# Optimization experiments

Hardware: AMD Instinct MI355X
Metric: run time of the kernel (lower is better)

## Reference

```python
import jax, jax.numpy as jnp
import numpy as np

B, D, N0, N1 = 2, 512, 2048, 2048
ATT_DIM, OUT_DIM, H = 512, 512, 8
HEAD_ATT = ATT_DIM // H   # 64
HEAD_OUT = OUT_DIM // H   # 64
TEMP = 1.0
MASK_FILL = -10000000.0


def setup_inputs() -> dict:
    key = jax.random.key(0)
    ks = jax.random.split(key, 12)
    s = 0.02
    return {
        "feats_query": jax.random.normal(ks[0], (B, D, N0), dtype=jnp.float32),
        "feats_key": jax.random.normal(ks[1], (B, D, N1), dtype=jnp.float32),
        "key_mask": jax.random.randint(ks[2], (B, 1, N1), 0, 2, dtype=jnp.int32),
        # 1x1 Conv1d weights == (out_ch, in_ch) matrices
        "Wq": jax.random.normal(ks[3], (ATT_DIM, D), dtype=jnp.float32) * s,
        "bq": jnp.zeros((ATT_DIM,), dtype=jnp.float32),
        "Wk": jax.random.normal(ks[4], (ATT_DIM, D), dtype=jnp.float32) * s,
        "bk": jnp.zeros((ATT_DIM,), dtype=jnp.float32),
        "Wf": jax.random.normal(ks[5], (OUT_DIM, D), dtype=jnp.float32) * s,
        "bf": jnp.zeros((OUT_DIM,), dtype=jnp.float32),
        "Wm": jax.random.normal(ks[6], (OUT_DIM, OUT_DIM), dtype=jnp.float32) * s,
        "bm": jnp.zeros((OUT_DIM,), dtype=jnp.float32),
        "ln_g": jnp.ones((OUT_DIM,), dtype=jnp.float32),
        "ln_b": jnp.zeros((OUT_DIM,), dtype=jnp.float32),
    }


def _conv1x1(W, b, x):  # x: (b, in, n) -> (b, out, n)
    return jnp.einsum('oi,bin->bon', W, x) + b[None, :, None]


def reference(feats_query, feats_key, key_mask, Wq, bq, Wk, bk, Wf, bf, Wm, bm, ln_g, ln_b):
    b = feats_query.shape[0]
    n0 = feats_query.shape[2]
    n1 = feats_key.shape[2]
    # projections; channel split is (head_dim, head_num) per torch reshape
    q = _conv1x1(Wq, bq, feats_query).reshape(b, HEAD_ATT, H, n0)
    k = _conv1x1(Wk, bk, feats_key).reshape(b, HEAD_ATT, H, n1)
    v = _conv1x1(Wf, bf, feats_key).reshape(b, HEAD_OUT, H, n1)
    # attention: scores scaled by head_att_dim ** 0.5 (dim = query.shape[1])
    scores = jnp.einsum('bdhn,bdhm->bhnm', q / TEMP, k) / (HEAD_ATT ** 0.5)
    mask = key_mask.reshape(b, 1, 1, n1)
    scores = jnp.where(mask == 0, MASK_FILL, scores)
    prob = jax.nn.softmax(scores, axis=-1)
    feats_out = jnp.einsum('bhnm,bdhm->bdhn', prob, v).reshape(b, HEAD_OUT * H, n0)
    feats_out = _conv1x1(Wm, bm, feats_out)
    feats_out = feats_out + feats_query  # skip connection
    # SpecialLayerNorm: layernorm over channel dim (permute 0,2,1 -> LN -> permute back)
    x = feats_out.transpose(0, 2, 1)  # (b, n0, c)
    mu = jnp.mean(x, axis=-1, keepdims=True)
    var = jnp.var(x, axis=-1, keepdims=True)
    x = (x - mu) / jnp.sqrt(var + 1e-5) * ln_g + ln_b
    return x.transpose(0, 2, 1)  # (b, c, n0)
```

## Files before the change

kernel.cpp:

```cpp
#include <hip/hip_runtime.h>
#include <hip/hip_bf16.h>


using bf16x8 = __attribute__((ext_vector_type(8))) __bf16;
using f32x4  = __attribute__((ext_vector_type(4))) float;
using f32x16 = __attribute__((ext_vector_type(16))) float;
using us8    = __attribute__((ext_vector_type(8))) unsigned short;
using u32x4  = __attribute__((ext_vector_type(4))) unsigned int;

__device__ __forceinline__ unsigned short f2b(float f) {
  unsigned int u = __builtin_bit_cast(unsigned int, f);
  u += 0x7fffu + ((u >> 16) & 1u);
  return (unsigned short)(u >> 16);
}
__device__ __forceinline__ float b2f(unsigned short s) {
  unsigned int u = ((unsigned int)s) << 16;
  return __builtin_bit_cast(float, u);
}
__device__ __forceinline__ unsigned int cvtpk(float lo, float hi) {
  unsigned int w;
  asm("v_cvt_pk_bf16_f32 %0, %1, %2" : "=v"(w) : "v"(lo), "v"(hi));
  return w;
}
__device__ __forceinline__ void gl_lds16(const void* g, void* l) {
  __builtin_amdgcn_global_load_lds((const __attribute__((address_space(1))) void*)g,
                                   (__attribute__((address_space(3))) void*)l, 16, 0, 0);
}

__global__ __launch_bounds__(256) void k_transpose(
    const float* __restrict__ fq, const float* __restrict__ fk,
    unsigned short* __restrict__ xqt, unsigned short* __restrict__ xkt)
{
  const int which = blockIdx.z >> 1;
  const int b = blockIdx.z & 1;
  const int i0 = blockIdx.y * 64, n0 = blockIdx.x * 64;
  const float* __restrict__ src = which ? fk : fq;
  unsigned short* __restrict__ dst = which ? xkt : xqt;
  __shared__ float tile[64][65];
  const int t = threadIdx.x;
  const int cl = t & 63, rw = t >> 6;
  #pragma unroll
  for (int rr = 0; rr < 16; ++rr) {
    int il = rr * 4 + rw;
    tile[il][cl] = src[((size_t)b * 512 + i0 + il) * 2048 + n0 + cl];
  }
  __syncthreads();
  #pragma unroll
  for (int rr = 0; rr < 16; ++rr) {
    int nl = rr * 4 + rw;
    dst[((size_t)b * 2048 + n0 + nl) * 512 + i0 + cl] = f2b(tile[cl][nl]);
  }
}

__global__ __launch_bounds__(256) void k_prepw(
    const float* __restrict__ Wq, const float* __restrict__ Wk,
    const float* __restrict__ Wf, const float* __restrict__ Wm,
    const int* __restrict__ mask,
    unsigned short* __restrict__ wqb, unsigned short* __restrict__ wkb,
    unsigned short* __restrict__ wfb, unsigned short* __restrict__ wmb,
    float* __restrict__ biasf)
{
  const int cp = blockIdx.x;
  const int mat = blockIdx.y;
  const int t = threadIdx.x;
  if (mat < 3) {
    const float* W = (mat == 0) ? Wq : (mat == 1) ? Wk : Wf;
    unsigned short* O = (mat == 0) ? wqb : (mat == 1) ? wkb : wfb;
    const int orig = (cp & 63) * 8 + (cp >> 6);
    for (int j = t; j < 512; j += 256)
      O[cp * 512 + j] = f2b(W[orig * 512 + j]);
  } else if (mat == 3) {
    for (int j = t; j < 512; j += 256) {
      int h = j >> 6, d = j & 63;
      wmb[cp * 512 + j] = f2b(Wm[cp * 512 + d * 8 + h]);
    }
  } else {
    if (cp < 16) {
      int i = cp * 256 + t;
      biasf[i] = mask[i] ? 0.f : -100000.f;
    }
  }
}

__device__ __forceinline__ void gemm_tile_128(
    const unsigned short* __restrict__ A,
    const unsigned short* __restrict__ Bt,
    f32x4 (&acc)[4][4])
{
  __shared__ __attribute__((aligned(16))) unsigned short As[128 * 64];
  __shared__ __attribute__((aligned(16))) unsigned short Bs[128 * 64];
  const int t = threadIdx.x;
  const int w = t >> 6, l = t & 63, q = l >> 4, m16 = l & 15;
  const int wm = w >> 1, wn = w & 1;
  const f32x4 fz = {0.f, 0.f, 0.f, 0.f};
  #pragma unroll
  for (int mf = 0; mf < 4; ++mf)
    #pragma unroll
    for (int nf = 0; nf < 4; ++nf) acc[mf][nf] = fz;

  for (int ks = 0; ks < 8; ++ks) {
    __syncthreads();
    #pragma unroll
    for (int i = 0; i < 4; ++i) {
      int s = i * 256 + t;
      int row = s >> 3, j = s & 7;
      int jj = j ^ (row & 7);
      *(us8*)&As[row * 64 + (jj << 3)] = *(const us8*)&A[(size_t)row * 512 + ks * 64 + j * 8];
      *(us8*)&Bs[row * 64 + (jj << 3)] = *(const us8*)&Bt[(size_t)row * 512 + ks * 64 + j * 8];
    }
    __syncthreads();
    #pragma unroll
    for (int kk = 0; kk < 2; ++kk) {
      bf16x8 av[4], bv[4];
      #pragma unroll
      for (int mf = 0; mf < 4; ++mf) {
        int row = wm * 64 + mf * 16 + m16;
        av[mf] = *(const bf16x8*)&As[row * 64 + (((kk * 4 + q) ^ (row & 7)) << 3)];
      }
      #pragma unroll
      for (int nf = 0; nf < 4; ++nf) {
        int row = wn * 64 + nf * 16 + m16;
        bv[nf] = *(const bf16x8*)&Bs[row * 64 + (((kk * 4 + q) ^ (row & 7)) << 3)];
      }
      #pragma unroll
      for (int mf = 0; mf < 4; ++mf)
        #pragma unroll
        for (int nf = 0; nf < 4; ++nf)
          acc[mf][nf] = __builtin_amdgcn_mfma_f32_16x16x32_bf16(av[mf], bv[nf], acc[mf][nf], 0, 0, 0);
    }
  }
}

__global__ __launch_bounds__(256) void k_proj(
    const unsigned short* __restrict__ xqt, const unsigned short* __restrict__ xkt,
    const unsigned short* __restrict__ wqp, const unsigned short* __restrict__ wkp,
    const unsigned short* __restrict__ wfp,
    const float* __restrict__ bq, const float* __restrict__ bk, const float* __restrict__ bfv,
    unsigned short* __restrict__ Qb, unsigned short* __restrict__ Kb, unsigned short* __restrict__ VTb)
{
  const int lid = blockIdx.x;
  const int orig = (lid & 7) * 48 + (lid >> 3);
  const int z = orig >> 6;
  const int bid = orig & 63;
  const int b = z / 3, proj = z % 3;
  const int t = threadIdx.x, w = t >> 6, l = t & 63, q = l >> 4, m16 = l & 15;
  const int wm = w >> 1, wn = w & 1;
  f32x4 acc[4][4];

  const unsigned short* A;
  const unsigned short* Bt;
  int mt, nt_;
  if (proj < 2) {
    mt = bid >> 2; nt_ = bid & 3;
    A  = (proj == 0 ? xqt : xkt) + (size_t)b * 2048 * 512 + (size_t)mt * 128 * 512;
    Bt = (proj == 0 ? wqp : wkp) + (size_t)nt_ * 128 * 512;
  } else {
    mt = bid & 3; nt_ = bid >> 2;
    A  = wfp + (size_t)mt * 128 * 512;
    Bt = xkt + (size_t)b * 2048 * 512 + (size_t)nt_ * 128 * 512;
  }
  gemm_tile_128(A, Bt, acc);

  const float QSCALE = 0.18033688011112042f;

  if (proj < 2) {
    const float* bias = (proj == 0) ? bq : bk;
    unsigned short* dst = (proj == 0) ? Qb : Kb;
    #pragma unroll
    for (int mf = 0; mf < 4; ++mf)
      #pragma unroll
      for (int nf = 0; nf < 4; ++nf)
        #pragma unroll
        for (int r = 0; r < 4; ++r) {
          int n  = mt * 128 + wm * 64 + mf * 16 + q * 4 + r;
          int cp = nt_ * 128 + wn * 64 + nf * 16 + m16;
          int h = cp >> 6, d = cp & 63;
          float v = acc[mf][nf][r] + bias[d * 8 + h];
          if (proj == 0) v *= QSCALE;
          dst[((size_t)(b * 8 + h) * 2048 + n) * 64 + d] = f2b(v);
        }
  } else {
    #pragma unroll
    for (int mf = 0; mf < 4; ++mf)
      #pragma unroll
      for (int nf = 0; nf < 4; ++nf)
        #pragma unroll
        for (int r = 0; r < 4; ++r) {
          int cp = mt * 128 + wm * 64 + mf * 16 + q * 4 + r;
          int n  = nt_ * 128 + wn * 64 + nf * 16 + m16;
          int h = cp >> 6, d = cp & 63;
          float v = acc[mf][nf][r] + bfv[d * 8 + h];
          VTb[((size_t)(b * 8 + h) * 64 + d) * 2048 + n] = f2b(v);
        }
  }
}

__global__ __launch_bounds__(256, 2) void k_attn2(
    const unsigned short* __restrict__ Qb, const unsigned short* __restrict__ Kb,
    const unsigned short* __restrict__ VTb, const float* __restrict__ biasf,
    unsigned short* __restrict__ OT)
{
  const int lid = blockIdx.x;
  const int orig = ((lid & 7) << 6) | (lid >> 3);
  const int bh = orig >> 5, b = bh >> 3, h = bh & 7;
  const int nt = orig & 31;
  const int t = threadIdx.x, w = t >> 6, l = t & 63;
  const int q31 = l & 31, hi = l >> 5;

  __shared__ __attribute__((aligned(16))) char lds_all[65536];
  char* kbuf = lds_all + w * 8192;
  char* vbuf = lds_all + 32768 + w * 8192;

  const unsigned short* Kp = Kb + (size_t)bh * (2048 * 64);
  const unsigned short* Vp = VTb + (size_t)bh * (64 * 2048);
  const float* brow = biasf + b * 2048;

  bf16x8 qfr[2][4];
  {
    const unsigned short* Qp = Qb + ((size_t)bh * 2048 + nt * 64) * 64;
    #pragma unroll
    for (int qf = 0; qf < 2; ++qf)
      #pragma unroll
      for (int tq = 0; tq < 4; ++tq)
        qfr[qf][tq] = *(const bf16x8*)&Qp[(qf * 32 + q31) * 64 + tq * 16 + hi * 8];
  }

  f32x16 oacc[2][2];
  #pragma unroll
  for (int i = 0; i < 2; ++i)
    #pragma unroll
    for (int j2 = 0; j2 < 2; ++j2)
      #pragma unroll
      for (int r = 0; r < 16; ++r) oacc[i][j2][r] = 0.f;
  float lpart[2] = {0.f, 0.f};

  const int kr3 = l >> 3, ks3 = l & 7;
  const int vr4 = l >> 2, vs2 = l & 3;

  {
    int kv0 = w * 32;
    #pragma unroll
    for (int j = 0; j < 4; ++j)
      gl_lds16(Kp + (size_t)(kv0 + j * 8 + kr3) * 64 + (ks3 ^ kr3) * 8, kbuf + j * 1024);
    #pragma unroll
    for (int j = 0; j < 4; ++j) {
      int d = j * 16 + vr4;
      gl_lds16(Vp + (size_t)d * 2048 + kv0 + (vs2 ^ (d & 3)) * 8, vbuf + j * 1024);
    }
  }

  #pragma unroll 2
  for (int i = 0; i < 16; ++i) {
    const int bufi = i & 1;
    const int kv0 = (w + 4 * i) * 32;

    float4 bias[4];
    #pragma unroll
    for (int g = 0; g < 4; ++g)
      bias[g] = *(const float4*)&brow[kv0 + g * 8 + hi * 4];

    if (i < 15) {
      const int kvn = (w + 4 * (i + 1)) * 32;
      char* kb2 = kbuf + (bufi ^ 1) * 4096;
      char* vb2 = vbuf + (bufi ^ 1) * 4096;
      #pragma unroll
      for (int j = 0; j < 4; ++j)
        gl_lds16(Kp + (size_t)(kvn + j * 8 + kr3) * 64 + (ks3 ^ kr3) * 8, kb2 + j * 1024);
      #pragma unroll
      for (int j = 0; j < 4; ++j) {
        int d = j * 16 + vr4;
        gl_lds16(Vp + (size_t)d * 2048 + kvn + (vs2 ^ (d & 3)) * 8, vb2 + j * 1024);
      }
      asm volatile("s_waitcnt vmcnt(8)" ::: "memory");
    } else {
      asm volatile("s_waitcnt vmcnt(0)" ::: "memory");
    }
    __builtin_amdgcn_sched_barrier(0);

    const char* kb = kbuf + bufi * 4096;
    const char* vb = vbuf + bufi * 4096;

    bf16x8 ak[4];
    #pragma unroll
    for (int tq = 0; tq < 4; ++tq)
      ak[tq] = *(const bf16x8*)(kb + q31 * 128 + ((((tq << 1) | hi) ^ (q31 & 7)) * 16));

    f32x16 sacc[2];
    #pragma unroll
    for (int qf = 0; qf < 2; ++qf)
      #pragma unroll
      for (int r = 0; r < 16; ++r) sacc[qf][r] = 0.f;
    #pragma unroll
    for (int tq = 0; tq < 4; ++tq) {
      sacc[0] = __builtin_amdgcn_mfma_f32_32x32x16_bf16(ak[tq], qfr[0][tq], sacc[0], 0, 0, 0);
      sacc[1] = __builtin_amdgcn_mfma_f32_32x32x16_bf16(ak[tq], qfr[1][tq], sacc[1], 0, 0, 0);
    }

    bf16x8 av[2][2];
    #pragma unroll
    for (int df = 0; df < 2; ++df)
      #pragma unroll
      for (int tt = 0; tt < 2; ++tt)
        av[df][tt] = *(const bf16x8*)(vb + (df * 32 + q31) * 64 + ((((tt << 1) | hi) ^ (q31 & 3)) * 16));

    #pragma unroll
    for (int qf = 0; qf < 2; ++qf) {
      float e[16];
      #pragma unroll
      for (int g = 0; g < 4; ++g) {
        e[g*4+0] = __builtin_amdgcn_exp2f(sacc[qf][g*4+0] + bias[g].x);
        e[g*4+1] = __builtin_amdgcn_exp2f(sacc[qf][g*4+1] + bias[g].y);
        e[g*4+2] = __builtin_amdgcn_exp2f(sacc[qf][g*4+2] + bias[g].z);
        e[g*4+3] = __builtin_amdgcn_exp2f(sacc[qf][g*4+3] + bias[g].w);
      }
      float s0 = 0.f;
      #pragma unroll
      for (int r = 0; r < 16; ++r) s0 += e[r];
      lpart[qf] += s0;

      unsigned int W[8];
      #pragma unroll
      for (int j = 0; j < 8; ++j) W[j] = cvtpk(e[2*j], e[2*j+1]);
      asm("v_permlane32_swap_b32 %0, %1" : "+v"(W[0]), "+v"(W[2]));
      asm("v_permlane32_swap_b32 %0, %1" : "+v"(W[1]), "+v"(W[3]));
      asm("v_permlane32_swap_b32 %0, %1" : "+v"(W[4]), "+v"(W[6]));
      asm("v_permlane32_swap_b32 %0, %1" : "+v"(W[5]), "+v"(W[7]));
      u32x4 lo4 = {W[0], W[1], W[2], W[3]};
      u32x4 hi4 = {W[4], W[5], W[6], W[7]};
      bf16x8 pb0 = __builtin_bit_cast(bf16x8, lo4);
      bf16x8 pb1 = __builtin_bit_cast(bf16x8, hi4);

      oacc[0][qf] = __builtin_amdgcn_mfma_f32_32x32x16_bf16(av[0][0], pb0, oacc[0][qf], 0, 0, 0);
      oacc[0][qf] = __builtin_amdgcn_mfma_f32_32x32x16_bf16(av[0][1], pb1, oacc[0][qf], 0, 0, 0);
      oacc[1][qf] = __builtin_amdgcn_mfma_f32_32x32x16_bf16(av[1][0], pb0, oacc[1][qf], 0, 0, 0);
      oacc[1][qf] = __builtin_amdgcn_mfma_f32_32x32x16_bf16(av[1][1], pb1, oacc[1][qf], 0, 0, 0);
    }
  }

  unsigned short* ot = (unsigned short*)kbuf;
  #pragma unroll
  for (int qf = 0; qf < 2; ++qf) {
    float ls = lpart[qf] + __shfl_xor(lpart[qf], 32);
    float rinv = __builtin_amdgcn_rcpf(ls);
    int qq = qf * 32 + q31;
    #pragma unroll
    for (int df = 0; df < 2; ++df)
      #pragma unroll
      for (int rg = 0; rg < 4; ++rg)
        #pragma unroll
        for (int pr = 0; pr < 2; ++pr) {
          int r0 = rg * 4 + pr * 2;
          unsigned int wv = cvtpk(oacc[df][qf][r0] * rinv, oacc[df][qf][r0 + 1] * rinv);
          *(unsigned int*)((char*)ot + qq * 128 + (((df * 4 + rg) ^ (qq & 7)) * 16) + hi * 8 + pr * 4) = wv;
        }
  }
  #pragma unroll
  for (int j = 0; j < 8; ++j) {
    int qq = j * 8 + (l >> 3);
    int sl = l & 7;
    us8 val = *(const us8*)((const char*)ot + qq * 128 + ((sl ^ (qq & 7)) * 16));
    *(us8*)&OT[((size_t)b * 2048 + nt * 64 + qq) * 512 + h * 64 + sl * 8] = val;
  }
}

__global__ __launch_bounds__(256) void k_out(
    const unsigned short* __restrict__ OT, const unsigned short* __restrict__ wmw,
    const float* __restrict__ bm, const unsigned short* __restrict__ xqt,
    const float* __restrict__ g, const float* __restrict__ be,
    float* __restrict__ out)
{
  const int b = blockIdx.y;
  const int n0 = blockIdx.x * 32;
  const int t = threadIdx.x, w = t >> 6, l = t & 63, q = l >> 4, m16 = l & 15;

  __shared__ __attribute__((aligned(16))) unsigned short As[32 * 64];
  __shared__ __attribute__((aligned(16))) unsigned short Bs[4][128 * 64];
  __shared__ float ssum[4][32], ssq[4][32];

  f32x4 acc[2][8];
  const f32x4 fz = {0.f, 0.f, 0.f, 0.f};
  #pragma unroll
  for (int mf = 0; mf < 2; ++mf)
    #pragma unroll
    for (int nf = 0; nf < 8; ++nf) acc[mf][nf] = fz;

  const unsigned short* Abase = OT + ((size_t)b * 2048 + n0) * 512;
  const unsigned short* Bbase = wmw + (size_t)w * 128 * 512;

  const int arow = t >> 3, aj = t & 7;
  for (int ks = 0; ks < 8; ++ks) {
    __syncthreads();
    gl_lds16(Abase + (size_t)arow * 512 + ks * 64 + ((aj ^ (arow & 7)) * 8),
             (char*)As + (size_t)w * 1024);
    #pragma unroll
    for (int c = 0; c < 16; ++c) {
      int slot = c * 64 + l;
      int row = slot >> 3, j = slot & 7;
      gl_lds16(Bbase + (size_t)row * 512 + ks * 64 + ((j ^ (row & 7)) * 8),
               (char*)Bs[w] + c * 1024);
    }
    asm volatile("s_waitcnt vmcnt(0)" ::: "memory");
    __syncthreads();
    #pragma unroll
    for (int kk = 0; kk < 2; ++kk) {
      bf16x8 av[2];
      #pragma unroll
      for (int mf = 0; mf < 2; ++mf) {
        int row = mf * 16 + m16;
        av[mf] = *(const bf16x8*)((const char*)As + row * 128 + (((kk * 4 + q) ^ (row & 7)) * 16));
      }
      #pragma unroll
      for (int nf = 0; nf < 8; ++nf) {
        int row = nf * 16 + m16;
        bf16x8 bv = *(const bf16x8*)((const char*)Bs[w] + row * 128 + (((kk * 4 + q) ^ (row & 7)) * 16));
        acc[0][nf] = __builtin_amdgcn_mfma_f32_16x16x32_bf16(av[0], bv, acc[0][nf], 0, 0, 0);
        acc[1][nf] = __builtin_amdgcn_mfma_f32_16x16x32_bf16(av[1], bv, acc[1][nf], 0, 0, 0);
      }
    }
  }

  float gv[8], bev[8], bmv[8];
  #pragma unroll
  for (int nf = 0; nf < 8; ++nf) {
    int c = w * 128 + nf * 16 + m16;
    gv[nf] = g[c]; bev[nf] = be[c]; bmv[nf] = bm[c];
  }
  #pragma unroll
  for (int mf = 0; mf < 2; ++mf)
    #pragma unroll
    for (int nf = 0; nf < 8; ++nf) {
      int c = w * 128 + nf * 16 + m16;
      #pragma unroll
      for (int r = 0; r < 4; ++r) {
        int n = n0 + mf * 16 + q * 4 + r;
        acc[mf][nf][r] += bmv[nf] + b2f(xqt[((size_t)b * 2048 + n) * 512 + c]);
      }
    }
  #pragma unroll
  for (int mf = 0; mf < 2; ++mf)
    #pragma unroll
    for (int r = 0; r < 4; ++r) {
      float ps = 0.f, pss = 0.f;
      #pragma unroll
      for (int nf = 0; nf < 8; ++nf) {
        float v = acc[mf][nf][r];
        ps += v; pss += v * v;
      }
      ps += __shfl_xor(ps, 1); pss += __shfl_xor(pss, 1);
      ps += __shfl_xor(ps, 2); pss += __shfl_xor(pss, 2);
      ps += __shfl_xor(ps, 4); pss += __shfl_xor(pss, 4);
      ps += __shfl_xor(ps, 8); pss += __shfl_xor(pss, 8);
      if (m16 == 0) {
        ssum[w][mf * 16 + q * 4 + r] = ps;
        ssq[w][mf * 16 + q * 4 + r] = pss;
      }
    }
  __syncthreads();
  #pragma unroll
  for (int mf = 0; mf < 2; ++mf)
    #pragma unroll
    for (int r = 0; r < 4; ++r) {
      int nl = mf * 16 + q * 4 + r;
      float S  = ssum[0][nl] + ssum[1][nl] + ssum[2][nl] + ssum[3][nl];
      float SS = ssq[0][nl] + ssq[1][nl] + ssq[2][nl] + ssq[3][nl];
      float mu = S * (1.f / 512.f);
      float var = SS * (1.f / 512.f) - mu * mu;
      float rstd = rsqrtf(var + 1e-5f);
      #pragma unroll
      for (int nf = 0; nf < 8; ++nf)
        acc[mf][nf][r] = (acc[mf][nf][r] - mu) * rstd * gv[nf] + bev[nf];
    }
  #pragma unroll
  for (int mf = 0; mf < 2; ++mf)
    #pragma unroll
    for (int nf = 0; nf < 8; ++nf) {
      int c = w * 128 + nf * 16 + m16;
      *(f32x4*)&out[((size_t)b * 512 + c) * 2048 + n0 + mf * 16 + q * 4] = acc[mf][nf];
    }
}

extern "C" void kernel_launch(void* const* d_in, const int* in_sizes, int n_in,
                              void* d_out, int out_size, void* d_ws, size_t ws_size,
                              hipStream_t stream) {
  const float* fq  = (const float*)d_in[0];
  const float* fk  = (const float*)d_in[1];
  const int*   msk = (const int*)d_in[2];
  const float* Wq  = (const float*)d_in[3];
  const float* bq  = (const float*)d_in[4];
  const float* Wk  = (const float*)d_in[5];
  const float* bk  = (const float*)d_in[6];
  const float* Wf  = (const float*)d_in[7];
  const float* bfv = (const float*)d_in[8];
  const float* Wm  = (const float*)d_in[9];
  const float* bm  = (const float*)d_in[10];
  const float* lng = (const float*)d_in[11];
  const float* lnb = (const float*)d_in[12];
  float* out = (float*)d_out;

  char* ws = (char*)d_ws;
  const size_t MB = 1024 * 1024;
  unsigned short* xqt = (unsigned short*)(ws + 0 * MB);
  unsigned short* xkt = (unsigned short*)(ws + 4 * MB);
  unsigned short* wqb = (unsigned short*)(ws + 8 * MB);
  unsigned short* wkb = (unsigned short*)(ws + 8 * MB + 512 * 1024);
  unsigned short* wfb = (unsigned short*)(ws + 9 * MB);
  unsigned short* wmb = (unsigned short*)(ws + 9 * MB + 512 * 1024);
  unsigned short* Qb  = (unsigned short*)(ws + 10 * MB);
  unsigned short* Kb  = (unsigned short*)(ws + 14 * MB);
  unsigned short* VTb = (unsigned short*)(ws + 18 * MB);
  unsigned short* OTb = (unsigned short*)(ws + 22 * MB);
  float*          biasf = (float*)(ws + 26 * MB);

  hipLaunchKernelGGL(k_transpose, dim3(32, 8, 4), dim3(256), 0, stream, fq, fk, xqt, xkt);
  hipLaunchKernelGGL(k_prepw, dim3(512, 5), dim3(256), 0, stream,
                     Wq, Wk, Wf, Wm, msk, wqb, wkb, wfb, wmb, biasf);
  hipLaunchKernelGGL(k_proj, dim3(384), dim3(256), 0, stream,
                     xqt, xkt, wqb, wkb, wfb, bq, bk, bfv, Qb, Kb, VTb);
  hipLaunchKernelGGL(k_attn2, dim3(512), dim3(256), 0, stream, Qb, Kb, VTb, biasf, OTb);
  hipLaunchKernelGGL(k_out, dim3(64, 2), dim3(256), 0, stream,
                     OTb, wmb, bm, xqt, lng, lnb, out);
}
```

Measured before the change: 74.71 us.

## Merge prep kernels, double-buffer proj/out GEMMs, raise MFMA priority, use fp32 residual

Merges the transpose and weight-prep kernels into one launch, which removes a launch and its dependency gap. The projection and output GEMMs now use double-buffered LDS filled by direct global-to-LDS loads, so the next K-slice loads while MFMAs run. The attention inner loop raises wave priority around its MFMA blocks. The output kernel reads the residual from the original fp32 query instead of the bf16 transposed copy, which improves accuracy but gives a less coalesced strided read. The larger LDS footprint in k_out (about 136KB) may limit occupancy.

```diff
diff --git a/kernel.cpp b/kernel.cpp
--- a/kernel.cpp
+++ b/kernel.cpp
@@ -27,106 +27,59 @@
                                    (__attribute__((address_space(3))) void*)l, 16, 0, 0);
 }
 
-__global__ __launch_bounds__(256) void k_transpose(
+__global__ __launch_bounds__(256) void k_pre(
     const float* __restrict__ fq, const float* __restrict__ fk,
-    unsigned short* __restrict__ xqt, unsigned short* __restrict__ xkt)
-{
-  const int which = blockIdx.z >> 1;
-  const int b = blockIdx.z & 1;
-  const int i0 = blockIdx.y * 64, n0 = blockIdx.x * 64;
-  const float* __restrict__ src = which ? fk : fq;
-  unsigned short* __restrict__ dst = which ? xkt : xqt;
-  __shared__ float tile[64][65];
-  const int t = threadIdx.x;
-  const int cl = t & 63, rw = t >> 6;
-  #pragma unroll
-  for (int rr = 0; rr < 16; ++rr) {
-    int il = rr * 4 + rw;
-    tile[il][cl] = src[((size_t)b * 512 + i0 + il) * 2048 + n0 + cl];
-  }
-  __syncthreads();
-  #pragma unroll
-  for (int rr = 0; rr < 16; ++rr) {
-    int nl = rr * 4 + rw;
-    dst[((size_t)b * 2048 + n0 + nl) * 512 + i0 + cl] = f2b(tile[cl][nl]);
-  }
-}
-
-__global__ __launch_bounds__(256) void k_prepw(
     const float* __restrict__ Wq, const float* __restrict__ Wk,
     const float* __restrict__ Wf, const float* __restrict__ Wm,
     const int* __restrict__ mask,
+    unsigned short* __restrict__ xqt, unsigned short* __restrict__ xkt,
     unsigned short* __restrict__ wqb, unsigned short* __restrict__ wkb,
     unsigned short* __restrict__ wfb, unsigned short* __restrict__ wmb,
     float* __restrict__ biasf)
 {
-  const int cp = blockIdx.x;
-  const int mat = blockIdx.y;
+  const int id = blockIdx.x;
   const int t = threadIdx.x;
-  if (mat < 3) {
-    const float* W = (mat == 0) ? Wq : (mat == 1) ? Wk : Wf;
-    unsigned short* O = (mat == 0) ? wqb : (mat == 1) ? wkb : wfb;
-    const int orig = (cp & 63) * 8 + (cp >> 6);
-    for (int j = t; j < 512; j += 256)
-      O[cp * 512 + j] = f2b(W[orig * 512 + j]);
-  } else if (mat == 3) {
-    for (int j = t; j < 512; j += 256) {
-      int h = j >> 6, d = j & 63;
-      wmb[cp * 512 + j] = f2b(Wm[cp * 512 + d * 8 + h]);
+  __shared__ float tile[64][65];
+
+  if (id < 1024) {
+    const int which = id >> 9;
+    const int b = (id >> 8) & 1;
+    const int i0 = ((id >> 5) & 7) * 64;
+    const int n0 = (id & 31) * 64;
+    const float* __restrict__ src = which ? fk : fq;
+    unsigned short* __restrict__ dst = which ? xkt : xqt;
+    const int cl = t & 63, rw = t >> 6;
+    #pragma unroll
+    for (int rr = 0; rr < 16; ++rr) {
+      int il = rr * 4 + rw;
+      tile[il][cl] = src[((size_t)b * 512 + i0 + il) * 2048 + n0 + cl];
+    }
+    __syncthreads();
+    #pragma unroll
+    for (int rr = 0; rr < 16; ++rr) {
+      int nl = rr * 4 + rw;
+      dst[((size_t)b * 2048 + n0 + nl) * 512 + i0 + cl] = f2b(tile[cl][nl]);
+    }
+  } else if (id < 3072) {
+    const int r = id - 1024;
+    const int mat = r >> 9, cp = r & 511;
+    if (mat < 3) {
+      const float* W = (mat == 0) ? Wq : (mat == 1) ? Wk : Wf;
+      unsigned short* O = (mat == 0) ? wqb : (mat == 1) ? wkb : wfb;
+      const int orig = (cp & 63) * 8 + (cp >> 6);
+      for (int j = t; j < 512; j += 256)
+        O[cp * 512 + j] = f2b(W[orig * 512 + j]);
+    } else {
+      for (int j = t; j < 512; j += 256) {
+        int h = j >> 6, d = j & 63;
+        wmb[cp * 512 + j] = f2b(Wm[cp * 512 + d * 8 + h]);
+      }
     }
   } else {
-    if (cp < 16) {
-      int i = cp * 256 + t;
+    const int r = id - 3072;
+    if (r < 16) {
+      int i = r * 256 + t;
       biasf[i] = mask[i] ? 0.f : -100000.f;
-    }
-  }
-}
-
-__device__ __forceinline__ void gemm_tile_128(
-    const unsigned short* __restrict__ A,
-    const unsigned short* __restrict__ Bt,
-    f32x4 (&acc)[4][4])
-{
-  __shared__ __attribute__((aligned(16))) unsigned short As[128 * 64];
-  __shared__ __attribute__((aligned(16))) unsigned short Bs[128 * 64];
-  const int t = threadIdx.x;
-  const int w = t >> 6, l = t & 63, q = l >> 4, m16 = l & 15;
-  const int wm = w >> 1, wn = w & 1;
-  const f32x4 fz = {0.f, 0.f, 0.f, 0.f};
-  #pragma unroll
-  for (int mf = 0; mf < 4; ++mf)
-    #pragma unroll
-    for (int nf = 0; nf < 4; ++nf) acc[mf][nf] = fz;
-
-  for (int ks = 0; ks < 8; ++ks) {
-    __syncthreads();
-    #pragma unroll
-    for (int i = 0; i < 4; ++i) {
-      int s = i * 256 + t;
-      int row = s >> 3, j = s & 7;
-      int jj = j ^ (row & 7);
-      *(us8*)&As[row * 64 + (jj << 3)] = *(const us8*)&A[(size_t)row * 512 + ks * 64 + j * 8];
-      *(us8*)&Bs[row * 64 + (jj << 3)] = *(const us8*)&Bt[(size_t)row * 512 + ks * 64 + j * 8];
-    }
-    __syncthreads();
-    #pragma unroll
-    for (int kk = 0; kk < 2; ++kk) {
-      bf16x8 av[4], bv[4];
-      #pragma unroll
-      for (int mf = 0; mf < 4; ++mf) {
-        int row = wm * 64 + mf * 16 + m16;
-        av[mf] = *(const bf16x8*)&As[row * 64 + (((kk * 4 + q) ^ (row & 7)) << 3)];
-      }
-      #pragma unroll
-      for (int nf = 0; nf < 4; ++nf) {
-        int row = wn * 64 + nf * 16 + m16;
-        bv[nf] = *(const bf16x8*)&Bs[row * 64 + (((kk * 4 + q) ^ (row & 7)) << 3)];
-      }
-      #pragma unroll
-      for (int mf = 0; mf < 4; ++mf)
-        #pragma unroll
-        for (int nf = 0; nf < 4; ++nf)
-          acc[mf][nf] = __builtin_amdgcn_mfma_f32_16x16x32_bf16(av[mf], bv[nf], acc[mf][nf], 0, 0, 0);
     }
   }
 }
@@ -145,7 +98,9 @@
   const int b = z / 3, proj = z % 3;
   const int t = threadIdx.x, w = t >> 6, l = t & 63, q = l >> 4, m16 = l & 15;
   const int wm = w >> 1, wn = w & 1;
-  f32x4 acc[4][4];
+
+  __shared__ __attribute__((aligned(16))) unsigned short As[2][8192];
+  __shared__ __attribute__((aligned(16))) unsigned short Bs[2][8192];
 
   const unsigned short* A;
   const unsigned short* Bt;
@@ -159,7 +114,60 @@
     A  = wfp + (size_t)mt * 128 * 512;
     Bt = xkt + (size_t)b * 2048 * 512 + (size_t)nt_ * 128 * 512;
   }
-  gemm_tile_128(A, Bt, acc);
+
+  f32x4 acc[4][4];
+  const f32x4 fz = {0.f, 0.f, 0.f, 0.f};
+  #pragma unroll
+  for (int mf = 0; mf < 4; ++mf)
+    #pragma unroll
+    for (int nf = 0; nf < 4; ++nf) acc[mf][nf] = fz;
+
+#define PROJ_STAGE(BUF, KS)                                                          \
+  {                                                                                  \
+    _Pragma("unroll")                                                                \
+    for (int c = 0; c < 4; ++c) {                                                    \
+      int slot = c * 256 + t;                                                        \
+      int row = slot >> 3, j = slot & 7;                                             \
+      int jj = j ^ (row & 7);                                                        \
+      gl_lds16(A  + (size_t)row * 512 + (KS) * 64 + jj * 8,                          \
+               (char*)As[BUF] + (c * 256 + w * 64) * 16);                            \
+      gl_lds16(Bt + (size_t)row * 512 + (KS) * 64 + jj * 8,                          \
+               (char*)Bs[BUF] + (c * 256 + w * 64) * 16);                            \
+    }                                                                                \
+  }
+
+  PROJ_STAGE(0, 0)
+  asm volatile("s_waitcnt vmcnt(0)" ::: "memory");
+  __syncthreads();
+
+  for (int ks = 0; ks < 8; ++ks) {
+    const int cur = ks & 1;
+    if (ks < 7) PROJ_STAGE(cur ^ 1, ks + 1)
+    #pragma unroll
+    for (int kk = 0; kk < 2; ++kk) {
+      bf16x8 av[4], bv[4];
+      #pragma unroll
+      for (int mf = 0; mf < 4; ++mf) {
+        int row = wm * 64 + mf * 16 + m16;
+        av[mf] = *(const bf16x8*)&As[cur][row * 64 + (((kk * 4 + q) ^ (row & 7)) << 3)];
+      }
+      #pragma unroll
+      for (int nf = 0; nf < 4; ++nf) {
+        int row = wn * 64 + nf * 16 + m16;
+        bv[nf] = *(const bf16x8*)&Bs[cur][row * 64 + (((kk * 4 + q) ^ (row & 7)) << 3)];
+      }
+      #pragma unroll
+      for (int mf = 0; mf < 4; ++mf)
+        #pragma unroll
+        for (int nf = 0; nf < 4; ++nf)
+          acc[mf][nf] = __builtin_amdgcn_mfma_f32_16x16x32_bf16(av[mf], bv[nf], acc[mf][nf], 0, 0, 0);
+    }
+    if (ks < 7) {
+      asm volatile("s_waitcnt vmcnt(0)" ::: "memory");
+      __syncthreads();
+    }
+  }
+#undef PROJ_STAGE
 
   const float QSCALE = 0.18033688011112042f;
 
@@ -290,11 +298,13 @@
     for (int qf = 0; qf < 2; ++qf)
       #pragma unroll
       for (int r = 0; r < 16; ++r) sacc[qf][r] = 0.f;
+    __builtin_amdgcn_s_setprio(1);
     #pragma unroll
     for (int tq = 0; tq < 4; ++tq) {
       sacc[0] = __builtin_amdgcn_mfma_f32_32x32x16_bf16(ak[tq], qfr[0][tq], sacc[0], 0, 0, 0);
       sacc[1] = __builtin_amdgcn_mfma_f32_32x32x16_bf16(ak[tq], qfr[1][tq], sacc[1], 0, 0, 0);
     }
+    __builtin_amdgcn_s_setprio(0);
 
     bf16x8 av[2][2];
     #pragma unroll
@@ -330,10 +340,12 @@
       bf16x8 pb0 = __builtin_bit_cast(bf16x8, lo4);
       bf16x8 pb1 = __builtin_bit_cast(bf16x8, hi4);
 
+      __builtin_amdgcn_s_setprio(1);
       oacc[0][qf] = __builtin_amdgcn_mfma_f32_32x32x16_bf16(av[0][0], pb0, oacc[0][qf], 0, 0, 0);
       oacc[0][qf] = __builtin_amdgcn_mfma_f32_32x32x16_bf16(av[0][1], pb1, oacc[0][qf], 0, 0, 0);
       oacc[1][qf] = __builtin_amdgcn_mfma_f32_32x32x16_bf16(av[1][0], pb0, oacc[1][qf], 0, 0, 0);
       oacc[1][qf] = __builtin_amdgcn_mfma_f32_32x32x16_bf16(av[1][1], pb1, oacc[1][qf], 0, 0, 0);
+      __builtin_amdgcn_s_setprio(0);
     }
   }
 
@@ -365,7 +377,7 @@
 
 __global__ __launch_bounds__(256) void k_out(
     const unsigned short* __restrict__ OT, const unsigned short* __restrict__ wmw,
-    const float* __restrict__ bm, const unsigned short* __restrict__ xqt,
+    const float* __restrict__ bm, const float* __restrict__ fq,
     const float* __restrict__ g, const float* __restrict__ be,
     float* __restrict__ out)
 {
@@ -373,8 +385,8 @@
   const int n0 = blockIdx.x * 32;
   const int t = threadIdx.x, w = t >> 6, l = t & 63, q = l >> 4, m16 = l & 15;
 
-  __shared__ __attribute__((aligned(16))) unsigned short As[32 * 64];
-  __shared__ __attribute__((aligned(16))) unsigned short Bs[4][128 * 64];
+  __shared__ __attribute__((aligned(16))) unsigned short As[2][2048];
+  __shared__ __attribute__((aligned(16))) unsigned short Bs[2][32768];
   __shared__ float ssum[4][32], ssq[4][32];
 
   f32x4 acc[2][8];
@@ -385,39 +397,51 @@
     for (int nf = 0; nf < 8; ++nf) acc[mf][nf] = fz;
 
   const unsigned short* Abase = OT + ((size_t)b * 2048 + n0) * 512;
-  const unsigned short* Bbase = wmw + (size_t)w * 128 * 512;
-
-  const int arow = t >> 3, aj = t & 7;
+  const unsigned short* Bbase = wmw;
+
+#define OUT_STAGE(BUF, KS)                                                          \
+  {                                                                                 \
+    { int row = t >> 3, j = t & 7;                                                  \
+      gl_lds16(Abase + (size_t)row * 512 + (KS) * 64 + ((j ^ (row & 7)) * 8),       \
+               (char*)As[BUF] + w * 1024); }                                        \
+    _Pragma("unroll")                                                               \
+    for (int c = 0; c < 16; ++c) {                                                  \
+      int slot = c * 256 + t;                                                       \
+      int row = slot >> 3, j = slot & 7;                                            \
+      gl_lds16(Bbase + (size_t)row * 512 + (KS) * 64 + ((j ^ (row & 7)) * 8),       \
+               (char*)Bs[BUF] + (c * 256 + w * 64) * 16);                           \
+    }                                                                               \
+  }
+
+  OUT_STAGE(0, 0)
+  asm volatile("s_waitcnt vmcnt(0)" ::: "memory");
+  __syncthreads();
+
   for (int ks = 0; ks < 8; ++ks) {
-    __syncthreads();
-    gl_lds16(Abase + (size_t)arow * 512 + ks * 64 + ((aj ^ (arow & 7)) * 8),
-             (char*)As + (size_t)w * 1024);
-    #pragma unroll
-    for (int c = 0; c < 16; ++c) {
-      int slot = c * 64 + l;
-      int row = slot >> 3, j = slot & 7;
-      gl_lds16(Bbase + (size_t)row * 512 + ks * 64 + ((j ^ (row & 7)) * 8),
-               (char*)Bs[w] + c * 1024);
-    }
-    asm volatile("s_waitcnt vmcnt(0)" ::: "memory");
-    __syncthreads();
+    const int cur = ks & 1;
+    if (ks < 7) OUT_STAGE(cur ^ 1, ks + 1)
     #pragma unroll
     for (int kk = 0; kk < 2; ++kk) {
       bf16x8 av[2];
       #pragma unroll
       for (int mf = 0; mf < 2; ++mf) {
         int row = mf * 16 + m16;
-        av[mf] = *(const bf16x8*)((const char*)As + row * 128 + (((kk * 4 + q) ^ (row & 7)) * 16));
+        av[mf] = *(const bf16x8*)((const char*)As[cur] + row * 128 + (((kk * 4 + q) ^ (row & 7)) * 16));
       }
       #pragma unroll
       for (int nf = 0; nf < 8; ++nf) {
-        int row = nf * 16 + m16;
-        bf16x8 bv = *(const bf16x8*)((const char*)Bs[w] + row * 128 + (((kk * 4 + q) ^ (row & 7)) * 16));
+        int row = w * 128 + nf * 16 + m16;
+        bf16x8 bv = *(const bf16x8*)((const char*)Bs[cur] + row * 128 + (((kk * 4 + q) ^ (row & 7)) * 16));
         acc[0][nf] = __builtin_amdgcn_mfma_f32_16x16x32_bf16(av[0], bv, acc[0][nf], 0, 0, 0);
         acc[1][nf] = __builtin_amdgcn_mfma_f32_16x16x32_bf16(av[1], bv, acc[1][nf], 0, 0, 0);
       }
     }
-  }
+    if (ks < 7) {
+      asm volatile("s_waitcnt vmcnt(0)" ::: "memory");
+      __syncthreads();
+    }
+  }
+#undef OUT_STAGE
 
   float gv[8], bev[8], bmv[8];
   #pragma unroll
@@ -430,11 +454,10 @@
     #pragma unroll
     for (int nf = 0; nf < 8; ++nf) {
       int c = w * 128 + nf * 16 + m16;
-      #pragma unroll
-      for (int r = 0; r < 4; ++r) {
-        int n = n0 + mf * 16 + q * 4 + r;
-        acc[mf][nf][r] += bmv[nf] + b2f(xqt[((size_t)b * 2048 + n) * 512 + c]);
-      }
+      f32x4 res = *(const f32x4*)&fq[((size_t)b * 512 + c) * 2048 + n0 + mf * 16 + q * 4];
+      #pragma unroll
+      for (int r = 0; r < 4; ++r)
+        acc[mf][nf][r] += bmv[nf] + res[r];
     }
   #pragma unroll
   for (int mf = 0; mf < 2; ++mf)
@@ -511,12 +534,11 @@
   unsigned short* OTb = (unsigned short*)(ws + 22 * MB);
   float*          biasf = (float*)(ws + 26 * MB);
 
-  hipLaunchKernelGGL(k_transpose, dim3(32, 8, 4), dim3(256), 0, stream, fq, fk, xqt, xkt);
-  hipLaunchKernelGGL(k_prepw, dim3(512, 5), dim3(256), 0, stream,
-                     Wq, Wk, Wf, Wm, msk, wqb, wkb, wfb, wmb, biasf);
+  hipLaunchKernelGGL(k_pre, dim3(3088), dim3(256), 0, stream,
+                     fq, fk, Wq, Wk, Wf, Wm, msk, xqt, xkt, wqb, wkb, wfb, wmb, biasf);
   hipLaunchKernelGGL(k_proj, dim3(384), dim3(256), 0, stream,
                      xqt, xkt, wqb, wkb, wfb, bq, bk, bfv, Qb, Kb, VTb);
   hipLaunchKernelGGL(k_attn2, dim3(512), dim3(256), 0, stream, Qb, Kb, VTb, biasf, OTb);
   hipLaunchKernelGGL(k_out, dim3(64, 2), dim3(256), 0, stream,
-                     OTb, wmb, bm, xqt, lng, lnb, out);
-}
+                     OTb, wmb, bm, fq, lng, lnb, out);
+}
```

Result: faster. 72.57 us (-2.9%).
